# Optimization experiments

Measured on AMD Instinct MI355X. Metric: run time of the kernel, lower is better.

Reference implementation:

```python
import jax, jax.numpy as jnp
import numpy as np


def _elem_mlp(x, w1, b1, w2, b2):
    # elementwise 1 -> N -> 1 ReLU MLP (distilled exp / inv approximators)
    h = jax.nn.relu(x[..., None] * w1[:, 0] + b1)  # [..., N]
    return jnp.einsum('...n,n->...', h, w2[0]) + b2[0]


def setup_inputs() -> dict:
    key = jax.random.key(0)
    ks = jax.random.split(key, 13)
    T, S, B, D = 8, 512, 8, 512
    NE, NI = 32, 64
    f = jnp.float32
    inp = {
        'sx': jax.random.normal(ks[0], (T, S, B, D), f) * 0.1,
        'q_proj_weight': jax.random.normal(ks[1], (D, D), f) / np.sqrt(D),
        'k_proj_weight': jax.random.normal(ks[2], (D, D), f) / np.sqrt(D),
        'q_proj_bias': jax.random.normal(ks[3], (D,), f) * 0.02,
        'k_proj_bias': jax.random.normal(ks[4], (D,), f) * 0.02,
        'exp_w1': jax.random.normal(ks[5], (NE, 1), f),
        'exp_b1': jax.random.normal(ks[6], (NE,), f) * 0.1,
        'exp_w2': jax.random.normal(ks[7], (1, NE), f) / np.sqrt(NE),
        'exp_b2': jax.random.normal(ks[8], (1,), f) * 0.01,
        'inv_w1': jax.random.normal(ks[9], (NI, 1), f),
        'inv_b1': jax.random.normal(ks[10], (NI,), f) * 0.1,
        'inv_w2': jax.random.normal(ks[11], (1, NI), f) / np.sqrt(NI),
        'inv_b2': jax.random.normal(ks[12], (1,), f) * 0.01,
        'num_heads': 8,
    }
    return inp


def reference(sx, q_proj_weight, k_proj_weight, q_proj_bias, k_proj_bias,
              exp_w1, exp_b1, exp_w2, exp_b2,
              inv_w1, inv_b1, inv_w2, inv_b2, num_heads):
    T, S, B, D = sx.shape
    H = num_heads
    hd = D // H
    scale = 1.0 / np.sqrt(hd)

    def proj(x_t, W, b):
        # [S, B, D] -> [B*H, S, hd]
        y = x_t @ W.T + b
        return y.reshape(S, B * H, hd).transpose(1, 0, 2)

    def step(carry, x_t):
        sum_q, sum_k, sum_p = carry
        sq = proj(x_t, q_proj_weight, q_proj_bias)
        sk = proj(x_t, k_proj_weight, k_proj_bias)
        sum_q = sum_q + sq
        # sp_t = sum_q @ sk^T + sq @ sum_k^T (sum_k updated AFTER, per snn_qk_product)
        sp = (jnp.einsum('bsh,bth->bst', sum_q, sk)
              + jnp.einsum('bsh,bth->bst', sq, sum_k)) * scale
        sum_k = sum_k + sk
        return (sum_q, sum_k, sum_p + sp), None

    z_qk = jnp.zeros((B * H, S, hd), sx.dtype)
    z_p = jnp.zeros((B * H, S, S), sx.dtype)
    (sum_q, sum_k, sum_p), _ = jax.lax.scan(step, (z_qk, z_qk, z_p), sx)

    p = sum_p / T  # time-averaged accumulated QK product

    # fit_softmax: distilled-MLP softmax approximation
    tmax = p[:, :, 0:1]
    tp = jnp.minimum(p - (tmax - 1.0), 3.0)
    x_up = jnp.where(tp > -20.0,
                     _elem_mlp(tp, exp_w1, exp_b1, exp_w2, exp_b2), 0.0)
    partition = x_up.sum(-1, keepdims=True)
    p_inv = _elem_mlp(partition, inv_w1, inv_b1, inv_w2, inv_b2)
    out = x_up * p_inv
    partition_p2 = out.sum(-1, keepdims=True)
    p_inv2 = _elem_mlp(partition_p2, inv_w1, inv_b1, inv_w2, inv_b2)
    out2 = jnp.where(partition_p2 > 1.5, out * p_inv2, out)
    return out2
```

## Files before the change

kernel.cpp:

```cpp
#include <hip/hip_runtime.h>


#define T_  8
#define NE_ 32
#define NI_ 64

#define LUT_N   2048
#define LUT_LO  -20.0f
#define LUT_HI  3.0f
#define LUT_INVW (LUT_N / (LUT_HI - LUT_LO))
#define LUT_W    ((LUT_HI - LUT_LO) / LUT_N)

typedef __attribute__((ext_vector_type(8))) short bf16x8;
typedef __attribute__((ext_vector_type(4))) float f32x4;
typedef __attribute__((ext_vector_type(4))) unsigned int u32x4;

#define XS_OFF 0u
#define WQ_OFF 2097152u
#define WK_OFF 2359296u
#define QB_OFF 2621440u
#define KB_OFF 4718592u
#define LUT_OFF 6815744u

__device__ inline unsigned short f2bf(float f) {
  union { float f; unsigned u; } v; v.f = f;
  unsigned r = v.u + 0x7FFFu + ((v.u >> 16) & 1u);
  return (unsigned short)(r >> 16);
}

__device__ inline void gload16(const void* g, void* l) {
  __builtin_amdgcn_global_load_lds(
      (const __attribute__((address_space(1))) void*)g,
      (__attribute__((address_space(3))) void*)l, 16, 0, 0);
}

__device__ inline bf16x8 lds_read_swz(const unsigned short* base, int row, int byteoff) {
  int addr = row * 128 + (byteoff ^ ((row & 7) << 4));
  return *(const bf16x8*)((const char*)base + addr);
}

__device__ inline float invmlp4(float x, const float* __restrict__ w1,
                                const float* __restrict__ b1,
                                const float* __restrict__ w2, float b2) {
  float a0 = b2, a1 = 0.f, a2 = 0.f, a3 = 0.f;
#pragma unroll
  for (int n = 0; n < NI_; n += 4) {
    a0 += w2[n + 0] * fmaxf(x * w1[n + 0] + b1[n + 0], 0.0f);
    a1 += w2[n + 1] * fmaxf(x * w1[n + 1] + b1[n + 1], 0.0f);
    a2 += w2[n + 2] * fmaxf(x * w1[n + 2] + b1[n + 2], 0.0f);
    a3 += w2[n + 3] * fmaxf(x * w1[n + 3] + b1[n + 3], 0.0f);
  }
  return (a0 + a1) + (a2 + a3);
}

__device__ inline float expmlp_exact(float t, const float* __restrict__ w1,
                                     const float* __restrict__ b1,
                                     const float* __restrict__ w2, float b2) {
  float a = b2;
#pragma unroll
  for (int n = 0; n < NE_; n++) a += w2[n] * fmaxf(t * w1[n] + b1[n], 0.0f);
  return a;
}

__global__ __launch_bounds__(256) void k_pre(
    const float* __restrict__ sx, const float* __restrict__ wq,
    const float* __restrict__ wk, const float* __restrict__ ew1,
    const float* __restrict__ eb1, const float* __restrict__ ew2,
    const float* __restrict__ eb2p,
    unsigned short* __restrict__ xs, unsigned short* __restrict__ wqb,
    unsigned short* __restrict__ wkb, float* __restrict__ lut) {
  int bx = blockIdx.x, tid = threadIdx.x;
  if (bx < 2048) {
    size_t i = ((size_t)bx * 256 + tid) * 4;
    f32x4 a = __builtin_nontemporal_load((const f32x4*)(sx + i));
#pragma unroll
    for (int t = 1; t < T_; t++) {
      f32x4 v = __builtin_nontemporal_load((const f32x4*)(sx + (size_t)t * 2097152 + i));
      a += v;
    }
    ushort4 o; o.x = f2bf(a[0]); o.y = f2bf(a[1]); o.z = f2bf(a[2]); o.w = f2bf(a[3]);
    *(ushort4*)(xs + i) = o;
  } else if (bx < 2560) {
    const float* src = (bx < 2304) ? wq : wk;
    unsigned short* dst = (bx < 2304) ? wqb : wkb;
    int base = (bx < 2304) ? 2048 : 2304;
    size_t i = ((size_t)(bx - base) * 256 + tid) * 4;
    float4 a = *(const float4*)(src + i);
    ushort4 o; o.x = f2bf(a.x); o.y = f2bf(a.y); o.z = f2bf(a.z); o.w = f2bf(a.w);
    *(ushort4*)(dst + i) = o;
  } else {
    int i = (bx - 2560) * 256 + tid;
    if (i <= LUT_N) {
      float t = fmaf((float)i, LUT_W, LUT_LO);
      lut[i] = expmlp_exact(t, ew1, eb1, ew2, eb2p[0]);
    }
  }
}

__global__ __launch_bounds__(256, 2) void k_proj(
    const unsigned short* __restrict__ xs, const unsigned short* __restrict__ wb,
    const float* __restrict__ bq, const float* __restrict__ bk,
    unsigned short* __restrict__ outb) {
  __shared__ unsigned short Sh[2][128 * 64];
  int tid = threadIdx.x;
  int lane = tid & 63, w = tid >> 6;
  int r0 = blockIdx.x * 128;
  int c0 = blockIdx.y * 128;
  int z = blockIdx.z;
  const unsigned short* W = wb + (size_t)z * 262144;
  const float* bias = z ? bk : bq;
  unsigned short* dst = outb + (size_t)z * 2097152;
  float sc = z ? 1.0f : (1.0f / 64.0f);

  int rgrp = lane >> 4, cl = lane & 15;
  int r0w = (w >> 1) * 64, c0w = (w & 1) * 64;

  f32x4 acc[4][4];
  f32x4 zero = {0.f, 0.f, 0.f, 0.f};
#pragma unroll
  for (int m = 0; m < 4; m++)
#pragma unroll
    for (int n = 0; n < 4; n++) acc[m][n] = zero;

  int rl = lane >> 3, slot = lane & 7;

  for (int kt = 0; kt < 8; kt++) {
    int k0 = kt * 64;
#pragma unroll
    for (int i = 0; i < 4; i++) {
      int chunk = w * 4 + i;
      int r = chunk * 8 + rl;
      int sw = (slot ^ (r & 7)) * 8;
      gload16(xs + (size_t)(r0 + r) * 512 + k0 + sw, (char*)Sh[0] + chunk * 1024);
      gload16(W + (size_t)(c0 + r) * 512 + k0 + sw, (char*)Sh[1] + chunk * 1024);
    }
    __syncthreads();
#pragma unroll
    for (int kb = 0; kb < 2; kb++) {
      bf16x8 af[4], bfr[4];
#pragma unroll
      for (int m = 0; m < 4; m++) af[m] = lds_read_swz(Sh[0], r0w + 16 * m + cl, kb * 64 + rgrp * 16);
#pragma unroll
      for (int n = 0; n < 4; n++) bfr[n] = lds_read_swz(Sh[1], c0w + 16 * n + cl, kb * 64 + rgrp * 16);
#pragma unroll
      for (int m = 0; m < 4; m++)
#pragma unroll
        for (int n = 0; n < 4; n++)
          acc[m][n] = __builtin_amdgcn_mfma_f32_16x16x32_bf16(af[m], bfr[n], acc[m][n], 0, 0, 0);
    }
    __syncthreads();
  }

  unsigned short* Os = &Sh[0][0];
#pragma unroll
  for (int n = 0; n < 4; n++) {
    int cgl = c0w + 16 * n + cl;
    float bv = 8.0f * bias[c0 + cgl];
    int h = cgl >> 6, dh = cgl & 63;
    int hh = dh >> 5, rg2 = (dh >> 3) & 3, jj = dh & 7;
#pragma unroll
    for (int m = 0; m < 4; m++) {
#pragma unroll
      for (int j = 0; j < 4; j++) {
        int rgl = r0w + 16 * m + rgrp * 4 + j;
        int sl = rgl >> 3, b = rgl & 7;
        Os[(((b * 2 + h) * 2 + hh) * 512) + (rg2 * 16 + sl) * 8 + jj] =
            f2bf((acc[m][n][j] + bv) * sc);
      }
    }
  }
  __syncthreads();

  int cb = r0 >> 7;
  int h0 = c0 >> 6;
#pragma unroll
  for (int i = 0; i < 8; i++) {
    int unit = i * 256 + tid;
    int b = unit >> 8, h = (unit >> 7) & 1, hh = (unit >> 6) & 1, inner = unit & 63;
    int bh = b * 8 + h0 + h;
    size_t du = ((size_t)((bh * 32 + cb) * 2 + hh)) * 512 + inner * 8;
    *(u32x4*)(dst + du) = *(const u32x4*)(Os + unit * 8);
  }
}

__global__ __launch_bounds__(256, 4) void k_attn(
    const unsigned short* __restrict__ qb, const unsigned short* __restrict__ kb,
    const float* __restrict__ lutg,
    const float* __restrict__ iw1, const float* __restrict__ ib1,
    const float* __restrict__ iw2, const float* __restrict__ ib2p,
    float* __restrict__ out) {
  __shared__ float Lut[LUT_N + 8];
  __shared__ float s_part[4][16];

  int tid = threadIdx.x;
  int lane = tid & 63, w = tid >> 6;
  int i = blockIdx.x;
  int xcd = i & 7, j2 = i >> 3;
  int bh = xcd * 8 + (j2 >> 5);
  int rb = j2 & 31;
  int rgrp = lane >> 4, cl = lane & 15;

#pragma unroll
  for (int c = 0; c < 2; c++) {
    int chunk = w * 2 + c;
    gload16((const char*)lutg + chunk * 1024 + lane * 16, (char*)Lut + chunk * 1024);
  }
  if (tid == 0) Lut[LUT_N] = lutg[LUT_N];

  const char* Qb = (const char*)qb + (size_t)((bh * 32 + rb) * 2) * 1024;
  bf16x8 aF0 = *(const bf16x8*)(Qb + lane * 16);
  bf16x8 aF1 = *(const bf16x8*)(Qb + 1024 + lane * 16);

  const char* Kbase = (const char*)kb + (size_t)(bh * 32) * 2048;
  f32x4 zero = {0.f, 0.f, 0.f, 0.f};

  float tm1[4];
  {
    bf16x8 b0 = *(const bf16x8*)(Kbase + lane * 16);
    bf16x8 b1 = *(const bf16x8*)(Kbase + 1024 + lane * 16);
    f32x4 p0 = __builtin_amdgcn_mfma_f32_16x16x32_bf16(aF0, b0, zero, 0, 0, 0);
    p0 = __builtin_amdgcn_mfma_f32_16x16x32_bf16(aF1, b1, p0, 0, 0, 0);
    int src = lane & 48;
#pragma unroll
    for (int j = 0; j < 4; j++) tm1[j] = __shfl(p0[j], src) - 1.0f;
  }

  f32x4 acc[8];
#pragma unroll
  for (int f = 0; f < 8; f++) {
    const char* Kb = Kbase + (size_t)(w * 8 + f) * 2048;
    bf16x8 b0 = *(const bf16x8*)(Kb + lane * 16);
    bf16x8 b1 = *(const bf16x8*)(Kb + 1024 + lane * 16);
    acc[f] = __builtin_amdgcn_mfma_f32_16x16x32_bf16(aF0, b0, zero, 0, 0, 0);
    acc[f] = __builtin_amdgcn_mfma_f32_16x16x32_bf16(aF1, b1, acc[f], 0, 0, 0);
  }

  __syncthreads();

  const float C0 = -LUT_LO * LUT_INVW;
  float rowsum[4] = {0.f, 0.f, 0.f, 0.f};
#pragma unroll
  for (int f = 0; f < 8; f++) {
#pragma unroll
    for (int j = 0; j < 4; j++) {
      float tp = fminf(acc[f][j] - tm1[j], 3.0f);
      float u = fmaxf(fmaf(tp, LUT_INVW, C0), 0.0f);
      int bi = (int)fminf(u, (float)(LUT_N - 1));
      float frac = u - (float)bi;
      float f0 = Lut[bi], f1 = Lut[bi + 1];
      float xu = fmaf(frac, f1 - f0, f0);
      xu = (tp > -20.0f) ? xu : 0.0f;
      acc[f][j] = xu;
      rowsum[j] += xu;
    }
  }

#pragma unroll
  for (int j = 0; j < 4; j++) {
    float s = rowsum[j];
    s += __shfl_xor(s, 1);
    s += __shfl_xor(s, 2);
    s += __shfl_xor(s, 4);
    s += __shfl_xor(s, 8);
    if (cl == 0) s_part[w][rgrp * 4 + j] = s;
  }
  __syncthreads();

  float fac;
  {
    int myrow = lane & 15;
    float part = s_part[0][myrow] + s_part[1][myrow] +
                 s_part[2][myrow] + s_part[3][myrow];
    float b2 = ib2p[0];
    fac = invmlp4(part, iw1, ib1, iw2, b2);
    float pp2 = part * fac;
    if (pp2 > 1.5f) fac *= invmlp4(pp2, iw1, ib1, iw2, b2);
  }

  float* outb = out + ((size_t)bh * 512 + rb * 16) * 512;
#pragma unroll
  for (int j = 0; j < 4; j++) {
    int row = rgrp * 4 + j;
    float fj = __shfl(fac, (lane & 48) | row);
#pragma unroll
    for (int f = 0; f < 8; f++)
      __builtin_nontemporal_store(acc[f][j] * fj,
          &outb[(size_t)row * 512 + w * 128 + 16 * f + cl]);
  }
}

extern "C" void kernel_launch(void* const* d_in, const int* in_sizes, int n_in,
                              void* d_out, int out_size, void* d_ws, size_t ws_size,
                              hipStream_t stream) {
  (void)in_sizes; (void)n_in; (void)out_size; (void)ws_size;
  const float* sx  = (const float*)d_in[0];
  const float* wq  = (const float*)d_in[1];
  const float* wk  = (const float*)d_in[2];
  const float* bq  = (const float*)d_in[3];
  const float* bk  = (const float*)d_in[4];
  const float* ew1 = (const float*)d_in[5];
  const float* eb1 = (const float*)d_in[6];
  const float* ew2 = (const float*)d_in[7];
  const float* eb2 = (const float*)d_in[8];
  const float* iw1 = (const float*)d_in[9];
  const float* ib1 = (const float*)d_in[10];
  const float* iw2 = (const float*)d_in[11];
  const float* ib2 = (const float*)d_in[12];
  unsigned short* wsu = (unsigned short*)d_ws;
  float* lut = (float*)(wsu + LUT_OFF);
  float* out = (float*)d_out;

  k_pre<<<2569, 256, 0, stream>>>(sx, wq, wk, ew1, eb1, ew2, eb2,
                                  wsu + XS_OFF, wsu + WQ_OFF, wsu + WK_OFF, lut);
  k_proj<<<dim3(32, 4, 2), 256, 0, stream>>>(wsu + XS_OFF, wsu + WQ_OFF, bq, bk, wsu + QB_OFF);
  k_attn<<<2048, 256, 0, stream>>>(wsu + QB_OFF, wsu + KB_OFF, lut,
                                   iw1, ib1, iw2, ib2, out);
}
```

Measured before the change: 62.85 us.

## Read paired LUT entries from global memory instead of staging in LDS

The exp lookup table is stored as float2 pairs (f(i), f(i+1)), so each lookup is one 8-byte global/L1 load rather than two LDS reads. The per-block LDS staging of the table and its barrier are removed, and the MFMA loop runs at raised wave priority. The LUT index math is folded into one FMA with a per-row constant. In exchange, lookups become data-dependent gathers through the cache hierarchy instead of LDS, and the table doubles in size.

Result: no change. 62.66 us (-0.3%).

```diff
diff --git a/kernel.cpp b/kernel.cpp
--- a/kernel.cpp
+++ b/kernel.cpp
@@ -68,7 +68,7 @@
     const float* __restrict__ eb1, const float* __restrict__ ew2,
     const float* __restrict__ eb2p,
     unsigned short* __restrict__ xs, unsigned short* __restrict__ wqb,
-    unsigned short* __restrict__ wkb, float* __restrict__ lut) {
+    unsigned short* __restrict__ wkb, float2* __restrict__ lut2) {
   int bx = blockIdx.x, tid = threadIdx.x;
   if (bx < 2048) {
     size_t i = ((size_t)bx * 256 + tid) * 4;
@@ -90,9 +90,12 @@
     *(ushort4*)(dst + i) = o;
   } else {
     int i = (bx - 2560) * 256 + tid;
-    if (i <= LUT_N) {
-      float t = fmaf((float)i, LUT_W, LUT_LO);
-      lut[i] = expmlp_exact(t, ew1, eb1, ew2, eb2p[0]);
+    if (i < LUT_N) {
+      float b2 = eb2p[0];
+      float tl = fmaf((float)i, LUT_W, LUT_LO);
+      float th = fmaf((float)(i + 1), LUT_W, LUT_LO);
+      lut2[i] = make_float2(expmlp_exact(tl, ew1, eb1, ew2, b2),
+                            expmlp_exact(th, ew1, eb1, ew2, b2));
     }
   }
 }
@@ -185,11 +188,10 @@
 
 __global__ __launch_bounds__(256, 4) void k_attn(
     const unsigned short* __restrict__ qb, const unsigned short* __restrict__ kb,
-    const float* __restrict__ lutg,
+    const float2* __restrict__ lut2,
     const float* __restrict__ iw1, const float* __restrict__ ib1,
     const float* __restrict__ iw2, const float* __restrict__ ib2p,
     float* __restrict__ out) {
-  __shared__ float Lut[LUT_N + 8];
   __shared__ float s_part[4][16];
 
   int tid = threadIdx.x;
@@ -200,13 +202,6 @@
   int rb = j2 & 31;
   int rgrp = lane >> 4, cl = lane & 15;
 
-#pragma unroll
-  for (int c = 0; c < 2; c++) {
-    int chunk = w * 2 + c;
-    gload16((const char*)lutg + chunk * 1024 + lane * 16, (char*)Lut + chunk * 1024);
-  }
-  if (tid == 0) Lut[LUT_N] = lutg[LUT_N];
-
   const char* Qb = (const char*)qb + (size_t)((bh * 32 + rb) * 2) * 1024;
   bf16x8 aF0 = *(const bf16x8*)(Qb + lane * 16);
   bf16x8 aF1 = *(const bf16x8*)(Qb + 1024 + lane * 16);
@@ -226,6 +221,7 @@
   }
 
   f32x4 acc[8];
+  __builtin_amdgcn_s_setprio(1);
 #pragma unroll
   for (int f = 0; f < 8; f++) {
     const char* Kb = Kbase + (size_t)(w * 8 + f) * 2048;
@@ -234,22 +230,25 @@
     acc[f] = __builtin_amdgcn_mfma_f32_16x16x32_bf16(aF0, b0, zero, 0, 0, 0);
     acc[f] = __builtin_amdgcn_mfma_f32_16x16x32_bf16(aF1, b1, acc[f], 0, 0, 0);
   }
-
-  __syncthreads();
+  __builtin_amdgcn_s_setprio(0);
 
   const float C0 = -LUT_LO * LUT_INVW;
+  float cj[4];
+#pragma unroll
+  for (int j = 0; j < 4; j++) cj[j] = fmaf(-tm1[j], LUT_INVW, C0);
+
   float rowsum[4] = {0.f, 0.f, 0.f, 0.f};
 #pragma unroll
   for (int f = 0; f < 8; f++) {
 #pragma unroll
     for (int j = 0; j < 4; j++) {
-      float tp = fminf(acc[f][j] - tm1[j], 3.0f);
-      float u = fmaxf(fmaf(tp, LUT_INVW, C0), 0.0f);
+      float u0 = fmaf(acc[f][j], LUT_INVW, cj[j]);
+      float u = fminf(fmaxf(u0, 0.0f), (float)LUT_N);
       int bi = (int)fminf(u, (float)(LUT_N - 1));
       float frac = u - (float)bi;
-      float f0 = Lut[bi], f1 = Lut[bi + 1];
-      float xu = fmaf(frac, f1 - f0, f0);
-      xu = (tp > -20.0f) ? xu : 0.0f;
+      float2 p2 = lut2[bi];
+      float xu = fmaf(frac, p2.y - p2.x, p2.x);
+      xu = (u0 > 0.0f) ? xu : 0.0f;
       acc[f][j] = xu;
       rowsum[j] += xu;
     }
@@ -307,12 +306,12 @@
   const float* iw2 = (const float*)d_in[11];
   const float* ib2 = (const float*)d_in[12];
   unsigned short* wsu = (unsigned short*)d_ws;
-  float* lut = (float*)(wsu + LUT_OFF);
+  float2* lut2 = (float2*)(wsu + LUT_OFF);
   float* out = (float*)d_out;
 
-  k_pre<<<2569, 256, 0, stream>>>(sx, wq, wk, ew1, eb1, ew2, eb2,
-                                  wsu + XS_OFF, wsu + WQ_OFF, wsu + WK_OFF, lut);
+  k_pre<<<2568, 256, 0, stream>>>(sx, wq, wk, ew1, eb1, ew2, eb2,
+                                  wsu + XS_OFF, wsu + WQ_OFF, wsu + WK_OFF, lut2);
   k_proj<<<dim3(32, 4, 2), 256, 0, stream>>>(wsu + XS_OFF, wsu + WQ_OFF, bq, bk, wsu + QB_OFF);
-  k_attn<<<2048, 256, 0, stream>>>(wsu + QB_OFF, wsu + KB_OFF, lut,
+  k_attn<<<2048, 256, 0, stream>>>(wsu + QB_OFF, wsu + KB_OFF, lut2,
                                    iw1, ib1, iw2, ib2, out);
 }
```
